# Kernel tuning notes

Hardware: AMD Instinct MI355X
Metric: run time of the kernel (lower is better)

## Reference

```python
import jax, jax.numpy as jnp
import numpy as np

B, T, N, E = 4, 30, 2000, 32000
F_IN, F_HID, F_GRU, N_CLS = 8, 64, 128, 2


def setup_inputs() -> dict:
    key = jax.random.key(0)
    ks = jax.random.split(key, 12)
    return {
        "x": jax.random.normal(ks[0], (B, T, N, F_IN), jnp.float32),
        "edge_index": jax.random.randint(ks[1], (B, T, 2, E), 0, N, jnp.int32),
        "W1": jax.random.normal(ks[2], (F_IN, F_HID), jnp.float32) * 0.1,
        "b1": jax.random.normal(ks[3], (F_HID,), jnp.float32) * 0.1,
        "W2": jax.random.normal(ks[4], (F_HID, F_HID), jnp.float32) * 0.1,
        "b2": jax.random.normal(ks[5], (F_HID,), jnp.float32) * 0.1,
        "W_ih": jax.random.normal(ks[6], (3 * F_GRU, F_HID), jnp.float32) * 0.1,
        "W_hh": jax.random.normal(ks[7], (3 * F_GRU, F_GRU), jnp.float32) * 0.1,
        "b_ih": jax.random.normal(ks[8], (3 * F_GRU,), jnp.float32) * 0.1,
        "b_hh": jax.random.normal(ks[9], (3 * F_GRU,), jnp.float32) * 0.1,
        "fc_w": jax.random.normal(ks[10], (N_CLS, F_GRU), jnp.float32) * 0.1,
        "fc_b": jax.random.normal(ks[11], (N_CLS,), jnp.float32) * 0.1,
    }


def _gcn_conv(x, src, dst, W, b):
    # PyG GCNConv (edge_weight=None): add self-loops, sym-normalize, x@W, scatter-add, +bias
    n = x.shape[0]
    loops = jnp.arange(n, dtype=src.dtype)
    s = jnp.concatenate([src, loops])
    d = jnp.concatenate([dst, loops])
    deg = jax.ops.segment_sum(jnp.ones(s.shape[0], x.dtype), d, num_segments=n)
    dis = jnp.where(deg > 0, jax.lax.rsqrt(deg), 0.0)
    norm = dis[s] * dis[d]                      # [E+N]
    h = x @ W                                   # [N, Fout]
    msg = h[s] * norm[:, None]                  # gather + scale
    return jax.ops.segment_sum(msg, d, num_segments=n) + b


def _frame_embed(x, ei, W1, b1, W2, b2):
    # one graph frame -> mean-pooled 64-d embedding
    src, dst = ei[0], ei[1]
    h = jax.nn.relu(_gcn_conv(x, src, dst, W1, b1))
    h = jax.nn.relu(_gcn_conv(h, src, dst, W2, b2))
    return h.mean(axis=0)


def _gru(H, W_ih, W_hh, b_ih, b_hh):
    # H: [T, B, F_HID]; torch GRU gate order: r, z, n
    def step(h, x_t):
        gi = x_t @ W_ih.T + b_ih                # [B, 3H]
        gh = h @ W_hh.T + b_hh
        i_r, i_z, i_n = jnp.split(gi, 3, axis=-1)
        h_r, h_z, h_n = jnp.split(gh, 3, axis=-1)
        r = jax.nn.sigmoid(i_r + h_r)
        z = jax.nn.sigmoid(i_z + h_z)
        n = jnp.tanh(i_n + r * h_n)
        h_new = (1.0 - z) * n + z * h
        return h_new, None
    h0 = jnp.zeros((H.shape[1], F_GRU), H.dtype)
    h_final, _ = jax.lax.scan(step, h0, H)
    return h_final                              # [B, F_GRU]


def reference(x, edge_index, W1, b1, W2, b2, W_ih, W_hh, b_ih, b_hh, fc_w, fc_b):
    G = B * T
    xf = x.reshape(G, N, F_IN)
    eif = edge_index.reshape(G, 2, E)
    emb = jax.vmap(_frame_embed, in_axes=(0, 0, None, None, None, None))(
        xf, eif, W1, b1, W2, b2)                # [G, 64]
    H = emb.reshape(B, T, F_HID).transpose(1, 0, 2)  # [T, B, 64]
    h_final = _gru(H, W_ih, W_hh, b_ih, b_hh)   # [B, 128]
    return h_final @ fc_w.T + fc_b              # [B, 2]
```

## Files before the change

kernel.cpp:

```cpp
#include <hip/hip_runtime.h>
#include <math.h>

#define G    120
#define Nn   2000
#define Ee   32000
#define Tt   30
#define Bb   4
#define Fg   128
#define QCAP 9216
#define TSLOT 48

static __device__ __forceinline__ unsigned short f2bf(float f) {
    unsigned u = __float_as_uint(f);
    u += 0x7fffu + ((u >> 16) & 1u);
    return (unsigned short)(u >> 16);
}

#if defined(__has_builtin)
#if __has_builtin(__builtin_amdgcn_cvt_f32_fp8) && __has_builtin(__builtin_amdgcn_cvt_pk_fp8_f32)
#define HW_FP8 1
#endif
#if __has_builtin(__builtin_amdgcn_cvt_pk_f32_fp8)
#define HW_FP8_PK 1
typedef float floatx2 __attribute__((ext_vector_type(2)));
#endif
#endif

static __device__ __forceinline__ unsigned fp8_enc_sw(float x) {
    unsigned s = (__float_as_uint(x) >> 24) & 0x80u;
    float ax = fminf(fabsf(x), 448.f);
    unsigned em;
    if (ax < 0.015625f) {
        em = (unsigned)__float2int_rn(ax * 512.f);
    } else {
        int e = (int)(__float_as_uint(ax) >> 23) - 127;
        float r = ax * __uint_as_float((unsigned)((130 - e) << 23));
        int q = __float2int_rn(r);
        em = (unsigned)(((e + 7) << 3) + (q - 8));
        em = min(em, 126u);
    }
    return s | em;
}
static __device__ __forceinline__ float fp8_dec_sw(unsigned b) {
    unsigned em = b & 0x7fu;
    float mag;
    if (em < 8u) mag = (float)em * 0.001953125f;
    else mag = __uint_as_float((((em >> 3) + 120u) << 23) | ((em & 7u) << 20));
    return (b & 0x80u) ? -mag : mag;
}
static __device__ __forceinline__ unsigned fp8_pack4(float a, float b, float c, float d) {
#ifdef HW_FP8
    int w = __builtin_amdgcn_cvt_pk_fp8_f32(a, b, 0, false);
    w = __builtin_amdgcn_cvt_pk_fp8_f32(c, d, w, true);
    return (unsigned)w;
#else
    return fp8_enc_sw(a) | (fp8_enc_sw(b) << 8) | (fp8_enc_sw(c) << 16) | (fp8_enc_sw(d) << 24);
#endif
}
static __device__ __forceinline__ void fp8x4_dec(unsigned dw, float* o) {
#ifdef HW_FP8_PK
    floatx2 lo = __builtin_amdgcn_cvt_pk_f32_fp8((int)dw, false);
    floatx2 hi = __builtin_amdgcn_cvt_pk_f32_fp8((int)dw, true);
    o[0] = lo[0]; o[1] = lo[1]; o[2] = hi[0]; o[3] = hi[1];
#else
    o[0] = fp8_dec_sw(dw & 0xffu);
    o[1] = fp8_dec_sw((dw >> 8) & 0xffu);
    o[2] = fp8_dec_sw((dw >> 16) & 0xffu);
    o[3] = fp8_dec_sw((dw >> 24) & 0xffu);
#endif
}

__global__ void __launch_bounds__(1024, 1)
k_bfuse(const int* __restrict__ ei, const float* __restrict__ x,
        const float* __restrict__ W1, const float* __restrict__ b1,
        const float* __restrict__ W2,
        float* __restrict__ dis, int* __restrict__ startA, int* __restrict__ csr,
        unsigned* __restrict__ ellT, int* __restrict__ cntS, int* __restrict__ ordS,
        float* __restrict__ emb, unsigned char* __restrict__ t2f) {
    __shared__ int   csr_l[Ee];
    __shared__ int   hist[Nn];
    __shared__ int   cntL[Nn];
    __shared__ int   nodeAt[Nn];
    __shared__ float disl[Nn];
    __shared__ int   dh[64];
    __shared__ int   db[64];
    __shared__ int   ovfS;
    int i = blockIdx.x;
    int g = i >> 1;
    int half = i & 1;
    int tid = threadIdx.x;
    for (int idx = tid; idx < Nn; idx += 1024) hist[idx] = 0;
    if (tid < 64) dh[tid] = 0;
    if (tid == 0) ovfS = 0;
    if (tid < 64) emb[g * 64 + tid] = 0.f;
    __syncthreads();
    const int* srcp = ei + (size_t)g * 2 * Ee;
    const int* dstp = srcp + Ee;
    for (int it = tid; it < Ee / 4; it += 1024) {
        int4 d = reinterpret_cast<const int4*>(dstp)[it];
        atomicAdd(&hist[d.x], 1);
        atomicAdd(&hist[d.y], 1);
        atomicAdd(&hist[d.z], 1);
        atomicAdd(&hist[d.w], 1);
    }
    __syncthreads();
    for (int idx = tid; idx < Nn; idx += 1024) {
        int c = hist[idx];
        cntL[idx] = c;
        float dv = rsqrtf((float)c + 1.0f);
        disl[idx] = dv;
        dis[(size_t)g * Nn + idx] = dv;
        atomicAdd(&dh[min(c, 63)], 1);
        if (c > TSLOT - 1) atomicMax(&ovfS, 1);
    }
    __syncthreads();
    for (int off = 1; off < Nn; off <<= 1) {
        int i1 = tid + 1024;
        int v0 = (tid >= off) ? hist[tid - off] : 0;
        int v1 = (i1 < Nn && i1 >= off) ? hist[i1 - off] : 0;
        __syncthreads();
        hist[tid] += v0;
        if (i1 < Nn) hist[i1] += v1;
        __syncthreads();
    }
    if (tid == 0) {
        int s = 0;
        for (int b = 0; b < 64; ++b) { db[b] = s; s += dh[b]; }
    }
    __syncthreads();
    if (tid < 64) dh[tid] = db[tid];
    __syncthreads();
    for (int idx = tid; idx < Nn; idx += 1024) {
        int p = atomicAdd(&dh[min(cntL[idx], 63)], 1);
        nodeAt[p] = idx;
        hist[idx] -= cntL[idx];
    }
    __syncthreads();
    for (int it = tid; it < Ee / 4; it += 1024) {
        int4 d = reinterpret_cast<const int4*>(dstp)[it];
        int4 s = reinterpret_cast<const int4*>(srcp)[it];
        csr_l[atomicAdd(&hist[d.x], 1)] = s.x;
        csr_l[atomicAdd(&hist[d.y], 1)] = s.y;
        csr_l[atomicAdd(&hist[d.z], 1)] = s.z;
        csr_l[atomicAdd(&hist[d.w], 1)] = s.w;
    }
    __syncthreads();
    if (tid < 1000) {
        int c = half * 1000 + tid;
        int n2 = nodeAt[c];
        int cnt2 = cntL[n2];
        int ex2 = hist[n2] - cnt2;
        size_t gc = (size_t)g * Nn + c;
        cntS[gc] = cnt2;
        ordS[gc] = n2;
        startA[(size_t)g * Nn + n2] = g * 4 * QCAP + ex2;
        float dn2 = disl[n2];
        unsigned* et = ellT + (size_t)g * TSLOT * Nn + c;
        et[0] = (unsigned)n2 | ((unsigned)f2bf(dn2 * dn2) << 16);
        int m2 = min(cnt2, TSLOT - 1);
        for (int e = 0; e < m2; ++e) {
            int s = csr_l[ex2 + e];
            et[(size_t)(e + 1) * Nn] = (unsigned)s | ((unsigned)f2bf(disl[s] * dn2) << 16);
        }
    }
    if (ovfS && half == 0) {
        int* cg = csr + (size_t)g * 4 * QCAP;
        for (int it = tid; it < Ee; it += 1024) cg[it] = csr_l[it];
    }
    __syncthreads();
    if (tid < 1000) {
        int c = half * 1000 + tid;
        int n = nodeAt[c];
        int cntn = cntL[n];
        int ex = hist[n] - cntn;
        float dn = disl[n];
        const float4* x4 = reinterpret_cast<const float4*>(x + (size_t)g * Nn * 8);
        float aX[8];
        {
            float w = dn * dn;
            float4 r0 = x4[n * 2], r1 = x4[n * 2 + 1];
            aX[0] = r0.x * w; aX[1] = r0.y * w; aX[2] = r0.z * w; aX[3] = r0.w * w;
            aX[4] = r1.x * w; aX[5] = r1.y * w; aX[6] = r1.z * w; aX[7] = r1.w * w;
        }
        for (int e0 = 0; e0 < cntn; e0 += 8) {
            int sb[8];
#pragma unroll
            for (int k2 = 0; k2 < 8; ++k2)
                sb[k2] = (e0 + k2 < cntn) ? csr_l[ex + e0 + k2] : -1;
#pragma unroll
            for (int k2 = 0; k2 < 8; ++k2) {
                if (sb[k2] >= 0) {
                    int s = sb[k2];
                    float w = disl[s] * dn;
                    float4 r0 = x4[s * 2], r1 = x4[s * 2 + 1];
                    aX[0] += r0.x * w; aX[1] += r0.y * w; aX[2] += r0.z * w; aX[3] += r0.w * w;
                    aX[4] += r1.x * w; aX[5] += r1.y * w; aX[6] += r1.z * w; aX[7] += r1.w * w;
                }
            }
        }
        float h1r[64];
        {
            const float4* b14 = reinterpret_cast<const float4*>(b1);
#pragma unroll
            for (int f4 = 0; f4 < 16; ++f4) {
                float4 b = b14[f4];
                h1r[4 * f4 + 0] = b.x; h1r[4 * f4 + 1] = b.y;
                h1r[4 * f4 + 2] = b.z; h1r[4 * f4 + 3] = b.w;
            }
            const float4* W14 = reinterpret_cast<const float4*>(W1);
#pragma unroll
            for (int k2 = 0; k2 < 8; ++k2) {
                float hk = aX[k2];
#pragma unroll
                for (int f4 = 0; f4 < 16; ++f4) {
                    float4 w = W14[k2 * 16 + f4];
                    h1r[4 * f4 + 0] += hk * w.x; h1r[4 * f4 + 1] += hk * w.y;
                    h1r[4 * f4 + 2] += hk * w.z; h1r[4 * f4 + 3] += hk * w.w;
                }
            }
#pragma unroll
            for (int f = 0; f < 64; ++f) h1r[f] = fmaxf(h1r[f], 0.f);
        }
        uint4 oh[2][2];
        {
            const float4* W24 = reinterpret_cast<const float4*>(W2);
#pragma unroll
            for (int hf = 0; hf < 2; ++hf) {
                float acch[32];
#pragma unroll
                for (int f = 0; f < 32; ++f) acch[f] = 0.f;
#pragma unroll
                for (int k2 = 0; k2 < 64; ++k2) {
                    float hk = h1r[k2];
#pragma unroll
                    for (int f4 = 0; f4 < 8; ++f4) {
                        float4 w = W24[k2 * 16 + hf * 8 + f4];
                        acch[4 * f4 + 0] += hk * w.x; acch[4 * f4 + 1] += hk * w.y;
                        acch[4 * f4 + 2] += hk * w.z; acch[4 * f4 + 3] += hk * w.w;
                    }
                }
                oh[hf][0].x = fp8_pack4(acch[0],  acch[1],  acch[2],  acch[3]);
                oh[hf][0].y = fp8_pack4(acch[4],  acch[5],  acch[6],  acch[7]);
                oh[hf][0].z = fp8_pack4(acch[8],  acch[9],  acch[10], acch[11]);
                oh[hf][0].w = fp8_pack4(acch[12], acch[13], acch[14], acch[15]);
                oh[hf][1].x = fp8_pack4(acch[16], acch[17], acch[18], acch[19]);
                oh[hf][1].y = fp8_pack4(acch[20], acch[21], acch[22], acch[23]);
                oh[hf][1].z = fp8_pack4(acch[24], acch[25], acch[26], acch[27]);
                oh[hf][1].w = fp8_pack4(acch[28], acch[29], acch[30], acch[31]);
            }
        }
        uint4* op = reinterpret_cast<uint4*>(t2f + ((size_t)g * Nn + n) * 64);
        op[0] = oh[0][0]; op[1] = oh[0][1]; op[2] = oh[1][0]; op[3] = oh[1][1];
    }
}

__global__ void __launch_bounds__(1024, 1)
k_aggF(const unsigned char* __restrict__ t2f, const unsigned* __restrict__ ellT,
       const int* __restrict__ cntS, const int* __restrict__ ordS,
       const int* __restrict__ startA, const int* __restrict__ csr,
       const float* __restrict__ dis, const float* __restrict__ bias,
       float* __restrict__ emb) {
    __shared__ uint4 stage[Nn * 5];
    int i = blockIdx.x;
    int xcd = i & 7;
    int j = i >> 3;
    int g = xcd * 15 + (j >> 1);
    int half = j & 1;
    int tid = threadIdx.x;
    int w = tid >> 6, lane = tid & 63;
    {
        const uint4* src = reinterpret_cast<const uint4*>(t2f + (size_t)g * Nn * 64);
        for (int it = tid; it < Nn * 4; it += 1024)
            stage[(it >> 2) * 5 + (it & 3)] = src[it];
    }
    __syncthreads();
#define ROWFMA(dw, base) { float o_[4]; fp8x4_dec(dw, o_); \
    acc[base + 0] += o_[0] * wt; acc[base + 1] += o_[1] * wt; \
    acc[base + 2] += o_[2] * wt; acc[base + 3] += o_[3] * wt; }
#define EDGEFMA(s, wt) { \
    uint4 r0 = stage[(s) * 5], r1 = stage[(s) * 5 + 1]; \
    uint4 r2 = stage[(s) * 5 + 2], r3 = stage[(s) * 5 + 3]; \
    ROWFMA(r0.x, 0)  ROWFMA(r0.y, 4)  ROWFMA(r0.z, 8)  ROWFMA(r0.w, 12) \
    ROWFMA(r1.x, 16) ROWFMA(r1.y, 20) ROWFMA(r1.z, 24) ROWFMA(r1.w, 28) \
    ROWFMA(r2.x, 32) ROWFMA(r2.y, 36) ROWFMA(r2.z, 40) ROWFMA(r2.w, 44) \
    ROWFMA(r3.x, 48) ROWFMA(r3.y, 52) ROWFMA(r3.z, 56) ROWFMA(r3.w, 60) }
    int po = w * 64 + lane;
    int p = half * 1000 + po;
    bool valid = (po < 1000);
    size_t gp = (size_t)g * Nn + (valid ? p : 0);
    int cnt = valid ? cntS[gp] : 0;
    int myc = valid ? (min(cnt, TSLOT - 1) + 1) : 0;
    float acc[64];
#pragma unroll
    for (int k = 0; k < 64; ++k) acc[k] = 0.f;
    const unsigned* et = ellT + (size_t)g * TSLOT * Nn + (valid ? p : 0);
    unsigned u_cur = (0 < myc) ? et[0] : 0u;
    for (int e = 0; e < TSLOT; ++e) {
        if (!__any(e < myc)) break;
        unsigned u_nxt = ((e + 1) < TSLOT && (e + 1) < myc)
                             ? et[(size_t)(e + 1) * Nn] : 0u;
        if (e < myc) {
            float wt = __uint_as_float(u_cur & 0xffff0000u);
            int s = u_cur & 0xffffu;
            EDGEFMA(s, wt)
        }
        u_cur = u_nxt;
    }
    if (cnt > TSLOT - 1) {
        int n = ordS[gp];
        size_t gn = (size_t)g * Nn + n;
        float dn = dis[gn];
        int start = startA[gn];
        const float* dsg = dis + (size_t)g * Nn;
        for (int e = TSLOT - 1; e < cnt; ++e) {
            int s = csr[start + e];
            float wt = dsg[s] * dn;
            EDGEFMA(s, wt)
        }
    }
#undef EDGEFMA
#undef ROWFMA
    float pool = 0.f;
#pragma unroll
    for (int k = 0; k < 64; ++k) {
        float v = valid ? fmaxf(acc[k] + bias[k], 0.f) : 0.f;
        v += __shfl_xor(v, 1);  v += __shfl_xor(v, 2);  v += __shfl_xor(v, 4);
        v += __shfl_xor(v, 8);  v += __shfl_xor(v, 16); v += __shfl_xor(v, 32);
        if (lane == k) pool = v;
    }
    atomicAdd(&emb[g * 64 + lane], pool * (1.0f / Nn));
}

__global__ void __launch_bounds__(768, 1)
k_gru_seq(const float* __restrict__ emb, const float* __restrict__ W_ih,
          const float* __restrict__ b_ih, const float* __restrict__ W_hh,
          const float* __restrict__ b_hh, const float* __restrict__ fc_w,
          const float* __restrict__ fc_b, float* __restrict__ out) {
    __shared__ float h[Fg];
    __shared__ float part[768];
    __shared__ float embs[Tt][64];
    __shared__ float pgi[Tt][768];
    int b = blockIdx.x;
    int tid = threadIdx.x;
    int row = tid >> 1;
    int half = tid & 1;
    float w[64];
    const float* wr = W_hh + (size_t)row * Fg + half * 64;
#pragma unroll
    for (int i = 0; i < 64; ++i) w[i] = wr[i];
    float wih[32];
    const float* wir = W_ih + (size_t)row * 64 + half * 32;
#pragma unroll
    for (int i = 0; i < 32; ++i) wih[i] = wir[i];
    for (int it = tid; it < Tt * 64; it += 768)
        embs[it >> 6][it & 63] = emb[((size_t)b * Tt) * 64 + it];
    if (tid < Fg) h[tid] = 0.f;
    __syncthreads();
    for (int t = 0; t < Tt; ++t) {
        const float* e = &embs[t][half * 32];
        float a0 = 0.f, a1 = 0.f, a2 = 0.f, a3 = 0.f;
#pragma unroll
        for (int i = 0; i < 8; ++i) {
            a0 += wih[4 * i + 0] * e[4 * i + 0];
            a1 += wih[4 * i + 1] * e[4 * i + 1];
            a2 += wih[4 * i + 2] * e[4 * i + 2];
            a3 += wih[4 * i + 3] * e[4 * i + 3];
        }
        pgi[t][tid] = (a0 + a1) + (a2 + a3);
    }
    __syncthreads();
    for (int t = 0; t < Tt; ++t) {
        const float* hh = &h[half * 64];
        float a0 = 0.f, a1 = 0.f, a2 = 0.f, a3 = 0.f;
#pragma unroll
        for (int i = 0; i < 16; ++i) {
            a0 += w[4 * i + 0] * hh[4 * i + 0];
            a1 += w[4 * i + 1] * hh[4 * i + 1];
            a2 += w[4 * i + 2] * hh[4 * i + 2];
            a3 += w[4 * i + 3] * hh[4 * i + 3];
        }
        part[tid] = (a0 + a1) + (a2 + a3);
        __syncthreads();
        if (tid < Fg) {
            int j = tid;
            float hr = b_hh[j]       + part[2 * j]           + part[2 * j + 1];
            float hz = b_hh[128 + j] + part[2 * (128 + j)]   + part[2 * (128 + j) + 1];
            float hn = b_hh[256 + j] + part[2 * (256 + j)]   + part[2 * (256 + j) + 1];
            float gr = b_ih[j]       + pgi[t][2 * j]         + pgi[t][2 * j + 1];
            float gz = b_ih[128 + j] + pgi[t][2 * (128 + j)] + pgi[t][2 * (128 + j) + 1];
            float gn = b_ih[256 + j] + pgi[t][2 * (256 + j)] + pgi[t][2 * (256 + j) + 1];
            float r  = 1.f / (1.f + expf(-(gr + hr)));
            float z  = 1.f / (1.f + expf(-(gz + hz)));
            float nn = tanhf(gn + r * hn);
            h[j] = (1.f - z) * nn + z * h[j];
        }
        __syncthreads();
    }
    if (tid < 2) {
        float acc = fc_b[tid];
        for (int k = 0; k < Fg; ++k) acc += fc_w[tid * Fg + k] * h[k];
        out[b * 2 + tid] = acc;
    }
}

extern "C" void kernel_launch(void* const* d_in, const int* in_sizes, int n_in,
                              void* d_out, int out_size, void* d_ws, size_t ws_size,
                              hipStream_t stream) {
    const float* x     = (const float*)d_in[0];
    const int*   ei    = (const int*)  d_in[1];
    const float* W1    = (const float*)d_in[2];
    const float* b1    = (const float*)d_in[3];
    const float* W2    = (const float*)d_in[4];
    const float* b2    = (const float*)d_in[5];
    const float* W_ih  = (const float*)d_in[6];
    const float* W_hh  = (const float*)d_in[7];
    const float* b_ih  = (const float*)d_in[8];
    const float* b_hh  = (const float*)d_in[9];
    const float* fc_w  = (const float*)d_in[10];
    const float* fc_b  = (const float*)d_in[11];
    float* out = (float*)d_out;

    char* ws = (char*)d_ws;
    size_t off = 0;
    auto alloc = [&](size_t bytes) -> void* {
        void* p = ws + off;
        off = (off + bytes + 255) & ~(size_t)255;
        return p;
    };
    float*    dis    = (float*)   alloc((size_t)G * Nn * 4);
    int*      startA = (int*)     alloc((size_t)G * Nn * 4);
    int*      cntS   = (int*)     alloc((size_t)G * Nn * 4);
    int*      ordS   = (int*)     alloc((size_t)G * Nn * 4);
    int*      csr    = (int*)     alloc((size_t)G * 4 * QCAP * 4);
    unsigned* ellT   = (unsigned*)alloc((size_t)G * TSLOT * Nn * 4);
    unsigned char* t2f = (unsigned char*)alloc((size_t)G * Nn * 64);
    float*    emb    = (float*)   alloc((size_t)G * 64 * 4);
    (void)ws_size; (void)in_sizes; (void)n_in; (void)out_size;

    hipLaunchKernelGGL(k_bfuse,   dim3(2 * G), dim3(1024), 0, stream,
                       ei, x, W1, b1, W2, dis, startA, csr, ellT, cntS, ordS, emb, t2f);
    hipLaunchKernelGGL(k_aggF,    dim3(240), dim3(1024), 0, stream, t2f, ellT, cntS, ordS, startA, csr, dis, b2, emb);
    hipLaunchKernelGGL(k_gru_seq, dim3(Bb), dim3(768), 0, stream, emb, W_ih, b_ih, W_hh, b_hh, fc_w, fc_b, out);
}
```

Baseline: 255.5 us.

## Fuse second GCN aggregation into build kernel via cooperative grid sync

Merges the aggregation kernel into the graph-build kernel using a cooperative launch and a grid-wide barrier. Each block then aggregates straight from its shared-memory CSR and degree arrays. This drops the ELL/CSR/dis/cnt workspace writes and rereads and one kernel launch. In exchange, neighbor rows are now read from global memory (L2) rather than staged in LDS, and 240 blocks of 1024 threads must all be co-resident for the grid sync to work.

```diff
diff --git a/kernel.cpp b/kernel.cpp
--- a/kernel.cpp
+++ b/kernel.cpp
@@ -1,4 +1,5 @@
 #include <hip/hip_runtime.h>
+#include <hip/hip_cooperative_groups.h>
 #include <math.h>
 
 #define G    120
@@ -7,8 +8,6 @@
 #define Tt   30
 #define Bb   4
 #define Fg   128
-#define QCAP 9216
-#define TSLOT 48
 
 static __device__ __forceinline__ unsigned short f2bf(float f) {
     unsigned u = __float_as_uint(f);
@@ -73,10 +72,8 @@
 __global__ void __launch_bounds__(1024, 1)
 k_bfuse(const int* __restrict__ ei, const float* __restrict__ x,
         const float* __restrict__ W1, const float* __restrict__ b1,
-        const float* __restrict__ W2,
-        float* __restrict__ dis, int* __restrict__ startA, int* __restrict__ csr,
-        unsigned* __restrict__ ellT, int* __restrict__ cntS, int* __restrict__ ordS,
-        float* __restrict__ emb, unsigned char* __restrict__ t2f) {
+        const float* __restrict__ W2, const float* __restrict__ b2,
+        unsigned char* __restrict__ t2f, float* __restrict__ emb) {
     __shared__ int   csr_l[Ee];
     __shared__ int   hist[Nn];
     __shared__ int   cntL[Nn];
@@ -84,14 +81,14 @@
     __shared__ float disl[Nn];
     __shared__ int   dh[64];
     __shared__ int   db[64];
-    __shared__ int   ovfS;
     int i = blockIdx.x;
-    int g = i >> 1;
-    int half = i & 1;
+    int xcd = i & 7;
+    int j = i >> 3;
+    int g = xcd * 15 + (j >> 1);
+    int half = j & 1;
     int tid = threadIdx.x;
     for (int idx = tid; idx < Nn; idx += 1024) hist[idx] = 0;
     if (tid < 64) dh[tid] = 0;
-    if (tid == 0) ovfS = 0;
     if (tid < 64) emb[g * 64 + tid] = 0.f;
     __syncthreads();
     const int* srcp = ei + (size_t)g * 2 * Ee;
@@ -107,11 +104,8 @@
     for (int idx = tid; idx < Nn; idx += 1024) {
         int c = hist[idx];
         cntL[idx] = c;
-        float dv = rsqrtf((float)c + 1.0f);
-        disl[idx] = dv;
-        dis[(size_t)g * Nn + idx] = dv;
+        disl[idx] = rsqrtf((float)c + 1.0f);
         atomicAdd(&dh[min(c, 63)], 1);
-        if (c > TSLOT - 1) atomicMax(&ovfS, 1);
     }
     __syncthreads();
     for (int off = 1; off < Nn; off <<= 1) {
@@ -143,29 +137,6 @@
         csr_l[atomicAdd(&hist[d.y], 1)] = s.y;
         csr_l[atomicAdd(&hist[d.z], 1)] = s.z;
         csr_l[atomicAdd(&hist[d.w], 1)] = s.w;
-    }
-    __syncthreads();
-    if (tid < 1000) {
-        int c = half * 1000 + tid;
-        int n2 = nodeAt[c];
-        int cnt2 = cntL[n2];
-        int ex2 = hist[n2] - cnt2;
-        size_t gc = (size_t)g * Nn + c;
-        cntS[gc] = cnt2;
-        ordS[gc] = n2;
-        startA[(size_t)g * Nn + n2] = g * 4 * QCAP + ex2;
-        float dn2 = disl[n2];
-        unsigned* et = ellT + (size_t)g * TSLOT * Nn + c;
-        et[0] = (unsigned)n2 | ((unsigned)f2bf(dn2 * dn2) << 16);
-        int m2 = min(cnt2, TSLOT - 1);
-        for (int e = 0; e < m2; ++e) {
-            int s = csr_l[ex2 + e];
-            et[(size_t)(e + 1) * Nn] = (unsigned)s | ((unsigned)f2bf(disl[s] * dn2) << 16);
-        }
-    }
-    if (ovfS && half == 0) {
-        int* cg = csr + (size_t)g * 4 * QCAP;
-        for (int it = tid; it < Ee; it += 1024) cg[it] = csr_l[it];
     }
     __syncthreads();
     if (tid < 1000) {
@@ -252,83 +223,56 @@
         uint4* op = reinterpret_cast<uint4*>(t2f + ((size_t)g * Nn + n) * 64);
         op[0] = oh[0][0]; op[1] = oh[0][1]; op[2] = oh[1][0]; op[3] = oh[1][1];
     }
-}
-
-__global__ void __launch_bounds__(1024, 1)
-k_aggF(const unsigned char* __restrict__ t2f, const unsigned* __restrict__ ellT,
-       const int* __restrict__ cntS, const int* __restrict__ ordS,
-       const int* __restrict__ startA, const int* __restrict__ csr,
-       const float* __restrict__ dis, const float* __restrict__ bias,
-       float* __restrict__ emb) {
-    __shared__ uint4 stage[Nn * 5];
-    int i = blockIdx.x;
-    int xcd = i & 7;
-    int j = i >> 3;
-    int g = xcd * 15 + (j >> 1);
-    int half = j & 1;
-    int tid = threadIdx.x;
-    int w = tid >> 6, lane = tid & 63;
+    cooperative_groups::this_grid().sync();
     {
-        const uint4* src = reinterpret_cast<const uint4*>(t2f + (size_t)g * Nn * 64);
-        for (int it = tid; it < Nn * 4; it += 1024)
-            stage[(it >> 2) * 5 + (it & 3)] = src[it];
-    }
-    __syncthreads();
+        int lane = tid & 63;
+        bool valid = (tid < 1000);
+        int c = half * 1000 + (valid ? tid : 0);
+        int n = nodeAt[c];
+        int cntn = valid ? cntL[n] : 0;
+        int ex = hist[n] - cntL[n];
+        float dn = disl[n];
+        const uint4* t4 = reinterpret_cast<const uint4*>(t2f + (size_t)g * Nn * 64);
+        float acc[64];
+#pragma unroll
+        for (int k = 0; k < 64; ++k) acc[k] = 0.f;
 #define ROWFMA(dw, base) { float o_[4]; fp8x4_dec(dw, o_); \
     acc[base + 0] += o_[0] * wt; acc[base + 1] += o_[1] * wt; \
     acc[base + 2] += o_[2] * wt; acc[base + 3] += o_[3] * wt; }
-#define EDGEFMA(s, wt) { \
-    uint4 r0 = stage[(s) * 5], r1 = stage[(s) * 5 + 1]; \
-    uint4 r2 = stage[(s) * 5 + 2], r3 = stage[(s) * 5 + 3]; \
+#define EDGEFMA(s, wv) { float wt = (wv); \
+    uint4 r0 = t4[(s) * 4], r1 = t4[(s) * 4 + 1]; \
+    uint4 r2 = t4[(s) * 4 + 2], r3 = t4[(s) * 4 + 3]; \
     ROWFMA(r0.x, 0)  ROWFMA(r0.y, 4)  ROWFMA(r0.z, 8)  ROWFMA(r0.w, 12) \
     ROWFMA(r1.x, 16) ROWFMA(r1.y, 20) ROWFMA(r1.z, 24) ROWFMA(r1.w, 28) \
     ROWFMA(r2.x, 32) ROWFMA(r2.y, 36) ROWFMA(r2.z, 40) ROWFMA(r2.w, 44) \
     ROWFMA(r3.x, 48) ROWFMA(r3.y, 52) ROWFMA(r3.z, 56) ROWFMA(r3.w, 60) }
-    int po = w * 64 + lane;
-    int p = half * 1000 + po;
-    bool valid = (po < 1000);
-    size_t gp = (size_t)g * Nn + (valid ? p : 0);
-    int cnt = valid ? cntS[gp] : 0;
-    int myc = valid ? (min(cnt, TSLOT - 1) + 1) : 0;
-    float acc[64];
-#pragma unroll
-    for (int k = 0; k < 64; ++k) acc[k] = 0.f;
-    const unsigned* et = ellT + (size_t)g * TSLOT * Nn + (valid ? p : 0);
-    unsigned u_cur = (0 < myc) ? et[0] : 0u;
-    for (int e = 0; e < TSLOT; ++e) {
-        if (!__any(e < myc)) break;
-        unsigned u_nxt = ((e + 1) < TSLOT && (e + 1) < myc)
-                             ? et[(size_t)(e + 1) * Nn] : 0u;
-        if (e < myc) {
-            float wt = __uint_as_float(u_cur & 0xffff0000u);
-            int s = u_cur & 0xffffu;
-            EDGEFMA(s, wt)
-        }
-        u_cur = u_nxt;
-    }
-    if (cnt > TSLOT - 1) {
-        int n = ordS[gp];
-        size_t gn = (size_t)g * Nn + n;
-        float dn = dis[gn];
-        int start = startA[gn];
-        const float* dsg = dis + (size_t)g * Nn;
-        for (int e = TSLOT - 1; e < cnt; ++e) {
-            int s = csr[start + e];
-            float wt = dsg[s] * dn;
-            EDGEFMA(s, wt)
-        }
-    }
+        if (valid) EDGEFMA(n, dn * dn)
+        for (int e0 = 0; ; e0 += 4) {
+            if (!__any(e0 < cntn)) break;
+            int sb[4];
+#pragma unroll
+            for (int k2 = 0; k2 < 4; ++k2)
+                sb[k2] = (e0 + k2 < cntn) ? csr_l[ex + e0 + k2] : -1;
+#pragma unroll
+            for (int k2 = 0; k2 < 4; ++k2) {
+                if (sb[k2] >= 0) {
+                    int s = sb[k2];
+                    EDGEFMA(s, disl[s] * dn)
+                }
+            }
+        }
 #undef EDGEFMA
 #undef ROWFMA
-    float pool = 0.f;
-#pragma unroll
-    for (int k = 0; k < 64; ++k) {
-        float v = valid ? fmaxf(acc[k] + bias[k], 0.f) : 0.f;
-        v += __shfl_xor(v, 1);  v += __shfl_xor(v, 2);  v += __shfl_xor(v, 4);
-        v += __shfl_xor(v, 8);  v += __shfl_xor(v, 16); v += __shfl_xor(v, 32);
-        if (lane == k) pool = v;
-    }
-    atomicAdd(&emb[g * 64 + lane], pool * (1.0f / Nn));
+        float pool = 0.f;
+#pragma unroll
+        for (int k = 0; k < 64; ++k) {
+            float v = valid ? fmaxf(acc[k] + b2[k], 0.f) : 0.f;
+            v += __shfl_xor(v, 1);  v += __shfl_xor(v, 2);  v += __shfl_xor(v, 4);
+            v += __shfl_xor(v, 8);  v += __shfl_xor(v, 16); v += __shfl_xor(v, 32);
+            if (lane == k) pool = v;
+        }
+        atomicAdd(&emb[g * 64 + lane], pool * (1.0f / Nn));
+    }
 }
 
 __global__ void __launch_bounds__(768, 1)
@@ -427,18 +371,14 @@
         off = (off + bytes + 255) & ~(size_t)255;
         return p;
     };
-    float*    dis    = (float*)   alloc((size_t)G * Nn * 4);
-    int*      startA = (int*)     alloc((size_t)G * Nn * 4);
-    int*      cntS   = (int*)     alloc((size_t)G * Nn * 4);
-    int*      ordS   = (int*)     alloc((size_t)G * Nn * 4);
-    int*      csr    = (int*)     alloc((size_t)G * 4 * QCAP * 4);
-    unsigned* ellT   = (unsigned*)alloc((size_t)G * TSLOT * Nn * 4);
     unsigned char* t2f = (unsigned char*)alloc((size_t)G * Nn * 64);
-    float*    emb    = (float*)   alloc((size_t)G * 64 * 4);
+    float*         emb = (float*)        alloc((size_t)G * 64 * 4);
     (void)ws_size; (void)in_sizes; (void)n_in; (void)out_size;
 
-    hipLaunchKernelGGL(k_bfuse,   dim3(2 * G), dim3(1024), 0, stream,
-                       ei, x, W1, b1, W2, dis, startA, csr, ellT, cntS, ordS, emb, t2f);
-    hipLaunchKernelGGL(k_aggF,    dim3(240), dim3(1024), 0, stream, t2f, ellT, cntS, ordS, startA, csr, dis, b2, emb);
-    hipLaunchKernelGGL(k_gru_seq, dim3(Bb), dim3(768), 0, stream, emb, W_ih, b_ih, W_hh, b_hh, fc_w, fc_b, out);
-}
+    void* args[] = { (void*)&ei, (void*)&x, (void*)&W1, (void*)&b1,
+                     (void*)&W2, (void*)&b2, (void*)&t2f, (void*)&emb };
+    hipLaunchCooperativeKernel((const void*)k_bfuse, dim3(2 * G), dim3(1024),
+                               args, 0, stream);
+    hipLaunchKernelGGL(k_gru_seq, dim3(Bb), dim3(768), 0, stream,
+                       emb, W_ih, b_ih, W_hh, b_hh, fc_w, fc_b, out);
+}
```

After: 424.4 us. +66.1%, slower.
